# Kernel optimization log

Measured on AMD Instinct MI355X. Metric: run time of the kernel, lower is better.

Reference implementation:

```python
import jax, jax.numpy as jnp
import numpy as np
import math

N_FEATURES = 64
GAMMA_ORDER = 0.5
ALPHA, BETA, ETA = 0.3, 0.4, 0.3
MAX_K = 50


def _make_coeffs():
    # gamma_values[0] = Gamma(g+1); gamma_values[m] (m>=1) = Gamma(m)*Gamma(g-m+2)
    g0 = math.gamma(GAMMA_ORDER + 1.0)
    coeffs = np.zeros(MAX_K + 1, dtype=np.float32)
    coeffs[0] = 1.0
    for k in range(1, MAX_K + 1):
        gv_k = math.gamma(k) * math.gamma(GAMMA_ORDER - k + 2.0)
        coeffs[k] = ((-1.0) ** k) * g0 / gv_k
    return jnp.asarray(coeffs)


def setup_inputs() -> dict:
    key = jax.random.key(0)
    k1, k2, k3, k4 = jax.random.split(key, 4)
    B, T, F = 4, 8192, N_FEATURES
    x = jax.random.normal(k1, (B, T, F), dtype=jnp.float32)
    weight_matrix = jax.random.normal(k2, (F, F), dtype=jnp.float32)
    bound = 1.0 / math.sqrt(F)
    proj_w = jax.random.uniform(k3, (F, F), dtype=jnp.float32, minval=-bound, maxval=bound)
    proj_b = jax.random.uniform(k4, (F,), dtype=jnp.float32, minval=-bound, maxval=bound)
    kappa = jnp.float32(0.1)
    coeffs = _make_coeffs()
    return {"x": x, "weight_matrix": weight_matrix, "proj_w": proj_w,
            "proj_b": proj_b, "kappa": kappa, "coeffs": coeffs}


def _fractional_derivative(x, coeffs):
    # causal conv: result[:, t, :] = sum_{k=0}^{min(t, max_k)} coeffs[k] * x[:, t-k, :]
    K = coeffs.shape[0]
    F = x.shape[-1]
    # depthwise 1D cross-correlation; kernel reversed so it implements x[t-k]
    kern = jnp.tile(coeffs[::-1][:, None, None], (1, 1, F))  # [K, 1, F]
    return jax.lax.conv_general_dilated(
        x, kern, window_strides=(1,), padding=[(K - 1, 0)],
        dimension_numbers=("NWC", "WIO", "NWC"), feature_group_count=F)


def reference(x, weight_matrix, proj_w, proj_b, kappa, coeffs):
    B, T, F = x.shape
    # 1) memory term: fractional derivative (causal conv)
    memory_term = _fractional_derivative(x, coeffs)

    # 2) coupling term: sum_j w[i,j] * tanh(x_i - x_j) * sigmoid(|x_i| + |x_j|)
    #    diagonal contributes tanh(0)=0, matching the i != j skip in the original.
    w = jax.nn.softmax(weight_matrix, axis=1)                 # [F, F]
    xi = x[..., :, None]                                      # [B, T, F, 1]
    xj = x[..., None, :]                                      # [B, T, 1, F]
    c = jnp.tanh(xi - xj) * jax.nn.sigmoid(jnp.abs(xi) + jnp.abs(xj))  # [B,T,F,F]
    coupling_term = jnp.einsum("btij,ij->bti", c, w)

    # 3) global term: proj(x[:, t]) * sum_{s=0}^{t} exp(-kappa * s)
    proj = x @ proj_w.T + proj_b                               # [B, T, F]
    kernel_cumsum = jnp.cumsum(jnp.exp(-kappa * jnp.arange(T, dtype=x.dtype)))
    global_term = proj * kernel_cumsum[None, :, None]

    output = ALPHA * memory_term + BETA * coupling_term + ETA * global_term
    return (output, memory_term)
```

## Files before the change

kernel.cpp:

```cpp
#include <hip/hip_runtime.h>
#include <hip/hip_fp16.h>
#include <math.h>

#define TT 8192
#define FF 64

typedef float f32x4 __attribute__((ext_vector_type(4)));

__device__ __forceinline__ float rcpf(float x) { return __builtin_amdgcn_rcpf(x); }

__global__ void prep_kernel(const float* __restrict__ W, const float* __restrict__ PW,
                            float* __restrict__ wsmT, float* __restrict__ pwT) {
    const int lane = threadIdx.x;
    const int wv   = threadIdx.y;
    for (int it = 0; it < 16; ++it) {
        const int r = wv * 16 + it;
        float v = W[r * 64 + lane];
        float m = v;
        #pragma unroll
        for (int off = 32; off >= 1; off >>= 1)
            m = fmaxf(m, __shfl_xor(m, off, 64));
        float e = __expf(v - m);
        float s = e;
        #pragma unroll
        for (int off = 32; off >= 1; off >>= 1)
            s += __shfl_xor(s, off, 64);
        wsmT[lane * 64 + r] = e * rcpf(s);
        pwT[lane * 64 + r]  = PW[r * 64 + lane];
    }
}

__global__ __launch_bounds__(256, 2)
void mcao_main(const float* __restrict__ x,
               const float* __restrict__ wsmT,
               const float* __restrict__ pwT,
               const float* __restrict__ pb,
               const float* __restrict__ kap,
               const float* __restrict__ coeffs,
               float* __restrict__ out,
               float* __restrict__ memout) {
    __shared__ __align__(16) char smem[66304];
    float*   xs  = (float*)smem;
    float*   tS  = (float*)smem;
    __half2* ux  = (__half2*)(smem + 16640);
    float*   P2  = (float*)(smem + 16640);
    float*   wS  = (float*)(smem + 33536);
    float*   pwS = (float*)(smem + 49920);

    const int tid  = threadIdx.x;
    const int lane = tid & 63;
    const int wv   = tid >> 6;

    const int sw = ((int)blockIdx.x & 7) * 64 + ((int)blockIdx.x >> 3);
    const int b  = sw >> 7;
    const int t0 = (sw & 127) * 64;
    const float* xb = x + (size_t)b * TT * FF;

    for (int i4 = tid; i4 < 114 * 16; i4 += 256) {
        const int s = i4 >> 4, f4 = i4 & 15, t = t0 - 50 + s;
        f32x4 v = {0.f, 0.f, 0.f, 0.f};
        if (t >= 0) v = *(const f32x4*)(xb + (size_t)t * 64 + f4 * 4);
        *(f32x4*)(&xs[i4 * 4]) = v;
    }
    #pragma unroll
    for (int k = 0; k < 4; ++k) {
        ((f32x4*)wS)[tid + 256 * k]  = ((const f32x4*)wsmT)[tid + 256 * k];
        ((f32x4*)pwS)[tid + 256 * k] = ((const f32x4*)pwT)[tid + 256 * k];
    }
    __syncthreads();

    float macc[16];
    #pragma unroll
    for (int r = 0; r < 16; ++r) macc[r] = 0.f;
    #pragma unroll
    for (int s = 0; s < 66; ++s) {
        const float xv = xs[(16 * wv + s) * 64 + lane];
        #pragma unroll
        for (int r = 0; r < 16; ++r) {
            const int k = r + 50 - s;
            if (0 <= k && k <= 50) macc[r] = fmaf(coeffs[k], xv, macc[r]);
        }
    }
    #pragma unroll
    for (int r = 0; r < 16; ++r)
        memout[(size_t)(b * TT + t0 + 16 * wv + r) * 64 + lane] = macc[r];

    const int prow = tid >> 2, pfq = tid & 3;
    float tq[16], uq[16], xq[16];
    #pragma unroll
    for (int c4 = 0; c4 < 4; ++c4) {
        const f32x4 xv4 = *(const f32x4*)(&xs[(50 + prow) * 64 + pfq * 16 + c4 * 4]);
        #pragma unroll
        for (int q = 0; q < 4; ++q) {
            const float xi = xv4[q];
            tq[c4 * 4 + q] = fmaf(-2.f, rcpf(__expf(2.f * xi) + 1.f), 1.f);
            uq[c4 * 4 + q] = __expf(-fabsf(xi));
            xq[c4 * 4 + q] = xi;
        }
    }
    __syncthreads();
    #pragma unroll
    for (int c = 0; c < 16; ++c) {
        const int f = pfq * 16 + c;
        tS[f * 65 + prow] = tq[c];
        ux[f * 66 + prow] = __floats2half2_rn(uq[c], xq[c]);
    }
    __syncthreads();

    const int i0 = wv * 16;
    float ti[16], ui[16];
    #pragma unroll
    for (int i = 0; i < 16; ++i) {
        ti[i] = tS[(i0 + i) * 65 + lane];
        ui[i] = __low2float(ux[(i0 + i) * 66 + lane]);
    }

    float cacc[16], pacc[16];
    #pragma unroll
    for (int i = 0; i < 16; ++i) { cacc[i] = 0.f; pacc[i] = 0.f; }

    #pragma unroll 4
    for (int j = 0; j < 64; ++j) {
        const float  tj  = tS[j * 65 + lane];
        const __half2 uxj = ux[j * 66 + lane];
        const float  ujf = __low2float(uxj);
        const float  xjf = __high2float(uxj);
        f32x4 w4[4], p4[4];
        #pragma unroll
        for (int q = 0; q < 4; ++q) {
            w4[q] = *(const f32x4*)(&wS[j * 64 + i0 + 4 * q]);
            p4[q] = *(const f32x4*)(&pwS[j * 64 + i0 + 4 * q]);
        }
        #pragma unroll
        for (int i = 0; i < 16; ++i) {
            const float wij = w4[i >> 2][i & 3];
            const float pij = p4[i >> 2][i & 3];
            const float d1 = fmaf(-ti[i], tj, 1.f);
            const float d2 = fmaf( ui[i], ujf, 1.f);
            const float rr = rcpf(d1 * d2);
            cacc[i] = fmaf((ti[i] - tj) * wij, rr, cacc[i]);
            pacc[i] = fmaf(xjf, pij, pacc[i]);
        }
    }

    const float kappa = kap[0];
    const float ksum  = (1.f - __expf(-kappa * (float)(t0 + lane + 1))) *
                        rcpf(1.f - __expf(-kappa));
    __syncthreads();
    #pragma unroll
    for (int i = 0; i < 16; ++i)
        P2[(i0 + i) * 65 + lane] =
            fmaf(0.4f, cacc[i], 0.3f * (pacc[i] + pb[i0 + i]) * ksum);
    __syncthreads();

    #pragma unroll
    for (int r = 0; r < 16; ++r) {
        const int row = 16 * wv + r;
        out[(size_t)(b * TT + t0 + row) * 64 + lane] =
            fmaf(0.3f, macc[r], P2[lane * 65 + row]);
    }
}

extern "C" void kernel_launch(void* const* d_in, const int* in_sizes, int n_in,
                              void* d_out, int out_size, void* d_ws, size_t ws_size,
                              hipStream_t stream) {
    const float* x   = (const float*)d_in[0];
    const float* W   = (const float*)d_in[1];
    const float* PW  = (const float*)d_in[2];
    const float* pb  = (const float*)d_in[3];
    const float* kap = (const float*)d_in[4];
    const float* cf  = (const float*)d_in[5];

    float* out    = (float*)d_out;
    float* memout = out + (size_t)4 * TT * FF;

    float* wsmT = (float*)d_ws;
    float* pwT  = wsmT + 64 * 64;

    hipLaunchKernelGGL(prep_kernel, dim3(1), dim3(64, 4), 0, stream, W, PW, wsmT, pwT);
    hipLaunchKernelGGL(mcao_main, dim3(4 * (TT / 64)), dim3(256), 0, stream,
                       x, wsmT, pwT, pb, kap, cf, out, memout);
}
```

Before: 50.59 us.

## Halve time tile to 32 rows and store weight matrices as fp16 in LDS

Cuts the time tile per block from 64 to 32 rows, which doubles the grid, and remaps threads so each wave covers 8 output features for 32 timesteps, using both wave halves. The softmax weights and projection weights are now stored as half precision, shrinking LDS use so four blocks fit per CU. The aim is more occupancy and parallelism, at the price of recomputing a relatively larger 50-row halo per tile and lower precision on the weights.

```diff
diff --git a/kernel.cpp b/kernel.cpp
--- a/kernel.cpp
+++ b/kernel.cpp
@@ -4,13 +4,15 @@
 
 #define TT 8192
 #define FF 64
+#define TILE 32
+#define HALO 50
 
 typedef float f32x4 __attribute__((ext_vector_type(4)));
 
 __device__ __forceinline__ float rcpf(float x) { return __builtin_amdgcn_rcpf(x); }
 
 __global__ void prep_kernel(const float* __restrict__ W, const float* __restrict__ PW,
-                            float* __restrict__ wsmT, float* __restrict__ pwT) {
+                            __half* __restrict__ wsmH, __half* __restrict__ pwH) {
     const int lane = threadIdx.x;
     const int wv   = threadIdx.y;
     for (int it = 0; it < 16; ++it) {
@@ -25,71 +27,69 @@
         #pragma unroll
         for (int off = 32; off >= 1; off >>= 1)
             s += __shfl_xor(s, off, 64);
-        wsmT[lane * 64 + r] = e * rcpf(s);
-        pwT[lane * 64 + r]  = PW[r * 64 + lane];
+        wsmH[lane * 64 + r] = __float2half(e * rcpf(s));
+        pwH[lane * 64 + r]  = __float2half(PW[r * 64 + lane]);
     }
 }
 
-__global__ __launch_bounds__(256, 2)
+__global__ __launch_bounds__(256, 4)
 void mcao_main(const float* __restrict__ x,
-               const float* __restrict__ wsmT,
-               const float* __restrict__ pwT,
+               const __half* __restrict__ wsmH,
+               const __half* __restrict__ pwH,
                const float* __restrict__ pb,
                const float* __restrict__ kap,
                const float* __restrict__ coeffs,
                float* __restrict__ out,
                float* __restrict__ memout) {
-    __shared__ __align__(16) char smem[66304];
+    __shared__ __align__(16) char smem[37376];
     float*   xs  = (float*)smem;
     float*   tS  = (float*)smem;
-    __half2* ux  = (__half2*)(smem + 16640);
-    float*   P2  = (float*)(smem + 16640);
-    float*   wS  = (float*)(smem + 33536);
-    float*   pwS = (float*)(smem + 49920);
+    __half2* ux  = (__half2*)(smem + 8448);
+    float*   P2  = (float*)smem;
+    __half*  wS  = (__half*)(smem + 20992);
+    __half*  pwS = (__half*)(smem + 29184);
 
     const int tid  = threadIdx.x;
     const int lane = tid & 63;
     const int wv   = tid >> 6;
 
-    const int sw = ((int)blockIdx.x & 7) * 64 + ((int)blockIdx.x >> 3);
-    const int b  = sw >> 7;
-    const int t0 = (sw & 127) * 64;
+    const int sw = ((int)blockIdx.x & 7) * 128 + ((int)blockIdx.x >> 3);
+    const int b  = sw >> 8;
+    const int t0 = (sw & 255) * TILE;
     const float* xb = x + (size_t)b * TT * FF;
 
-    for (int i4 = tid; i4 < 114 * 16; i4 += 256) {
-        const int s = i4 >> 4, f4 = i4 & 15, t = t0 - 50 + s;
+    for (int i4 = tid; i4 < (TILE + HALO) * 16; i4 += 256) {
+        const int s = i4 >> 4, f4 = i4 & 15, t = t0 - HALO + s;
         f32x4 v = {0.f, 0.f, 0.f, 0.f};
         if (t >= 0) v = *(const f32x4*)(xb + (size_t)t * 64 + f4 * 4);
         *(f32x4*)(&xs[i4 * 4]) = v;
     }
     #pragma unroll
-    for (int k = 0; k < 4; ++k) {
-        ((f32x4*)wS)[tid + 256 * k]  = ((const f32x4*)wsmT)[tid + 256 * k];
-        ((f32x4*)pwS)[tid + 256 * k] = ((const f32x4*)pwT)[tid + 256 * k];
+    for (int k = 0; k < 2; ++k) {
+        ((f32x4*)wS)[tid + 256 * k]  = ((const f32x4*)wsmH)[tid + 256 * k];
+        ((f32x4*)pwS)[tid + 256 * k] = ((const f32x4*)pwH)[tid + 256 * k];
     }
     __syncthreads();
 
-    float macc[16];
+    float macc[8] = {0.f,0.f,0.f,0.f,0.f,0.f,0.f,0.f};
     #pragma unroll
-    for (int r = 0; r < 16; ++r) macc[r] = 0.f;
-    #pragma unroll
-    for (int s = 0; s < 66; ++s) {
-        const float xv = xs[(16 * wv + s) * 64 + lane];
+    for (int s = 0; s < 58; ++s) {
+        const float xv = xs[(8 * wv + s) * 64 + lane];
         #pragma unroll
-        for (int r = 0; r < 16; ++r) {
+        for (int r = 0; r < 8; ++r) {
             const int k = r + 50 - s;
             if (0 <= k && k <= 50) macc[r] = fmaf(coeffs[k], xv, macc[r]);
         }
     }
     #pragma unroll
-    for (int r = 0; r < 16; ++r)
-        memout[(size_t)(b * TT + t0 + 16 * wv + r) * 64 + lane] = macc[r];
+    for (int r = 0; r < 8; ++r)
+        memout[(size_t)(b * TT + t0 + 8 * wv + r) * 64 + lane] = macc[r];
 
-    const int prow = tid >> 2, pfq = tid & 3;
-    float tq[16], uq[16], xq[16];
+    const int prow = tid >> 3, pfq = tid & 7;
+    float tq[8], uq[8], xq[8];
     #pragma unroll
-    for (int c4 = 0; c4 < 4; ++c4) {
-        const f32x4 xv4 = *(const f32x4*)(&xs[(50 + prow) * 64 + pfq * 16 + c4 * 4]);
+    for (int c4 = 0; c4 < 2; ++c4) {
+        const f32x4 xv4 = *(const f32x4*)(&xs[(HALO + prow) * 64 + pfq * 8 + c4 * 4]);
         #pragma unroll
         for (int q = 0; q < 4; ++q) {
             const float xi = xv4[q];
@@ -100,64 +100,60 @@
     }
     __syncthreads();
     #pragma unroll
-    for (int c = 0; c < 16; ++c) {
-        const int f = pfq * 16 + c;
-        tS[f * 65 + prow] = tq[c];
-        ux[f * 66 + prow] = __floats2half2_rn(uq[c], xq[c]);
+    for (int c = 0; c < 8; ++c) {
+        const int f = pfq * 8 + c;
+        tS[f * 33 + prow] = tq[c];
+        ux[f * 34 + prow] = __floats2half2_rn(uq[c], xq[c]);
     }
     __syncthreads();
 
-    const int i0 = wv * 16;
-    float ti[16], ui[16];
+    const int r  = lane & 31;
+    const int h  = lane >> 5;
+    const int ib = wv * 16 + h * 8;
+    float ti[8], ui[8];
     #pragma unroll
-    for (int i = 0; i < 16; ++i) {
-        ti[i] = tS[(i0 + i) * 65 + lane];
-        ui[i] = __low2float(ux[(i0 + i) * 66 + lane]);
+    for (int q = 0; q < 8; ++q) {
+        ti[q] = tS[(ib + q) * 33 + r];
+        ui[q] = __low2float(ux[(ib + q) * 34 + r]);
     }
 
-    float cacc[16], pacc[16];
-    #pragma unroll
-    for (int i = 0; i < 16; ++i) { cacc[i] = 0.f; pacc[i] = 0.f; }
-
-    #pragma unroll 4
+    float cacc[8] = {0,0,0,0,0,0,0,0};
+    float pacc[8] = {0,0,0,0,0,0,0,0};
+    #pragma unroll 8
     for (int j = 0; j < 64; ++j) {
-        const float  tj  = tS[j * 65 + lane];
-        const __half2 uxj = ux[j * 66 + lane];
+        const float  tj  = tS[j * 33 + r];
+        const __half2 uxj = ux[j * 34 + r];
         const float  ujf = __low2float(uxj);
         const float  xjf = __high2float(uxj);
-        f32x4 w4[4], p4[4];
+        __half wh[8], ph[8];
+        *(f32x4*)wh = *(const f32x4*)(wS  + j * 64 + ib);
+        *(f32x4*)ph = *(const f32x4*)(pwS + j * 64 + ib);
         #pragma unroll
-        for (int q = 0; q < 4; ++q) {
-            w4[q] = *(const f32x4*)(&wS[j * 64 + i0 + 4 * q]);
-            p4[q] = *(const f32x4*)(&pwS[j * 64 + i0 + 4 * q]);
-        }
-        #pragma unroll
-        for (int i = 0; i < 16; ++i) {
-            const float wij = w4[i >> 2][i & 3];
-            const float pij = p4[i >> 2][i & 3];
-            const float d1 = fmaf(-ti[i], tj, 1.f);
-            const float d2 = fmaf( ui[i], ujf, 1.f);
+        for (int q = 0; q < 8; ++q) {
+            const float d1 = fmaf(-ti[q], tj, 1.f);
+            const float d2 = fmaf( ui[q], ujf, 1.f);
             const float rr = rcpf(d1 * d2);
-            cacc[i] = fmaf((ti[i] - tj) * wij, rr, cacc[i]);
-            pacc[i] = fmaf(xjf, pij, pacc[i]);
+            const float s  = (ti[q] - tj) * rr;
+            cacc[q] = fmaf(__half2float(wh[q]), s,   cacc[q]);
+            pacc[q] = fmaf(__half2float(ph[q]), xjf, pacc[q]);
         }
     }
 
     const float kappa = kap[0];
-    const float ksum  = (1.f - __expf(-kappa * (float)(t0 + lane + 1))) *
+    const float ksum  = (1.f - __expf(-kappa * (float)(t0 + r + 1))) *
                         rcpf(1.f - __expf(-kappa));
     __syncthreads();
     #pragma unroll
-    for (int i = 0; i < 16; ++i)
-        P2[(i0 + i) * 65 + lane] =
-            fmaf(0.4f, cacc[i], 0.3f * (pacc[i] + pb[i0 + i]) * ksum);
+    for (int q = 0; q < 8; ++q)
+        P2[(ib + q) * 33 + r] =
+            fmaf(0.4f, cacc[q], 0.3f * (pacc[q] + pb[ib + q]) * ksum);
     __syncthreads();
 
     #pragma unroll
-    for (int r = 0; r < 16; ++r) {
-        const int row = 16 * wv + r;
+    for (int rr = 0; rr < 8; ++rr) {
+        const int row = 8 * wv + rr;
         out[(size_t)(b * TT + t0 + row) * 64 + lane] =
-            fmaf(0.3f, macc[r], P2[lane * 65 + row]);
+            fmaf(0.3f, macc[rr], P2[lane * 33 + row]);
     }
 }
 
@@ -174,10 +170,10 @@
     float* out    = (float*)d_out;
     float* memout = out + (size_t)4 * TT * FF;
 
-    float* wsmT = (float*)d_ws;
-    float* pwT  = wsmT + 64 * 64;
+    __half* wsmH = (__half*)d_ws;
+    __half* pwH  = wsmH + 64 * 64;
 
-    hipLaunchKernelGGL(prep_kernel, dim3(1), dim3(64, 4), 0, stream, W, PW, wsmT, pwT);
-    hipLaunchKernelGGL(mcao_main, dim3(4 * (TT / 64)), dim3(256), 0, stream,
-                       x, wsmT, pwT, pb, kap, cf, out, memout);
+    hipLaunchKernelGGL(prep_kernel, dim3(1), dim3(64, 4), 0, stream, W, PW, wsmH, pwH);
+    hipLaunchKernelGGL(mcao_main, dim3(4 * (TT / TILE)), dim3(256), 0, stream,
+                       x, wsmH, pwH, pb, kap, cf, out, memout);
 }
```

After: 54.10 us. 7.0% more time.

## Use 1024-thread blocks with 4 rows per wave and packed FP32 math

Applied to the files above, without the earlier changes.

Each 64-row tile is now split across 16 waves instead of 4, so every wave handles 4 output features and 4 time rows. This cuts per-thread register use and raises occupancy for the coupling loop. The coupling loop now uses packed two-wide FMAs, and tanh plus packed half-precision u/x values share one interleaved shared-memory layout, so a single 8-byte load fetches them together. In exchange, the causal convolution re-reads more halo rows per output row (54 loads per 4 rows instead of 66 per 16), and the launch-bounds hint asks for more resident waves than the hardware can hold.

```diff
diff --git a/kernel.cpp b/kernel.cpp
--- a/kernel.cpp
+++ b/kernel.cpp
@@ -4,7 +4,10 @@
 
 #define TT 8192
 #define FF 64
+#define TILE 64
+#define HALO 50
 
+typedef float f32x2 __attribute__((ext_vector_type(2)));
 typedef float f32x4 __attribute__((ext_vector_type(4)));
 
 __device__ __forceinline__ float rcpf(float x) { return __builtin_amdgcn_rcpf(x); }
@@ -30,7 +33,7 @@
     }
 }
 
-__global__ __launch_bounds__(256, 2)
+__global__ __launch_bounds__(1024, 8)
 void mcao_main(const float* __restrict__ x,
                const float* __restrict__ wsmT,
                const float* __restrict__ pwT,
@@ -39,13 +42,12 @@
                const float* __restrict__ coeffs,
                float* __restrict__ out,
                float* __restrict__ memout) {
-    __shared__ __align__(16) char smem[66304];
-    float*   xs  = (float*)smem;
-    float*   tS  = (float*)smem;
-    __half2* ux  = (__half2*)(smem + 16640);
-    float*   P2  = (float*)(smem + 16640);
-    float*   wS  = (float*)(smem + 33536);
-    float*   pwS = (float*)(smem + 49920);
+    __shared__ __align__(16) char smem[66048];
+    float* xs  = (float*)smem;
+    f32x2* tux = (f32x2*)smem;
+    float* P2  = (float*)smem;
+    float* wS  = (float*)(smem + 33280);
+    float* pwS = (float*)(smem + 49664);
 
     const int tid  = threadIdx.x;
     const int lane = tid & 63;
@@ -53,111 +55,113 @@
 
     const int sw = ((int)blockIdx.x & 7) * 64 + ((int)blockIdx.x >> 3);
     const int b  = sw >> 7;
-    const int t0 = (sw & 127) * 64;
+    const int t0 = (sw & 127) * TILE;
     const float* xb = x + (size_t)b * TT * FF;
 
-    for (int i4 = tid; i4 < 114 * 16; i4 += 256) {
-        const int s = i4 >> 4, f4 = i4 & 15, t = t0 - 50 + s;
-        f32x4 v = {0.f, 0.f, 0.f, 0.f};
-        if (t >= 0) v = *(const f32x4*)(xb + (size_t)t * 64 + f4 * 4);
-        *(f32x4*)(&xs[i4 * 4]) = v;
+    #pragma unroll
+    for (int k = 0; k < 2; ++k) {
+        const int i4 = tid + 1024 * k;
+        if (i4 < 114 * 16) {
+            const int s = i4 >> 4, f4 = i4 & 15, t = t0 - HALO + s;
+            f32x4 v = {0.f, 0.f, 0.f, 0.f};
+            if (t >= 0) v = *(const f32x4*)(xb + (size_t)t * 64 + f4 * 4);
+            *(f32x4*)(&xs[s * 64 + f4 * 4]) = v;
+        }
     }
-    #pragma unroll
-    for (int k = 0; k < 4; ++k) {
-        ((f32x4*)wS)[tid + 256 * k]  = ((const f32x4*)wsmT)[tid + 256 * k];
-        ((f32x4*)pwS)[tid + 256 * k] = ((const f32x4*)pwT)[tid + 256 * k];
-    }
+    ((f32x4*)wS)[tid]  = ((const f32x4*)wsmT)[tid];
+    ((f32x4*)pwS)[tid] = ((const f32x4*)pwT)[tid];
     __syncthreads();
 
-    float macc[16];
+    float macc[4] = {0.f, 0.f, 0.f, 0.f};
     #pragma unroll
-    for (int r = 0; r < 16; ++r) macc[r] = 0.f;
-    #pragma unroll
-    for (int s = 0; s < 66; ++s) {
-        const float xv = xs[(16 * wv + s) * 64 + lane];
+    for (int s = 0; s < 54; ++s) {
+        const float xv = xs[(4 * wv + s) * 64 + lane];
         #pragma unroll
-        for (int r = 0; r < 16; ++r) {
+        for (int r = 0; r < 4; ++r) {
             const int k = r + 50 - s;
             if (0 <= k && k <= 50) macc[r] = fmaf(coeffs[k], xv, macc[r]);
         }
     }
     #pragma unroll
-    for (int r = 0; r < 16; ++r)
-        memout[(size_t)(b * TT + t0 + 16 * wv + r) * 64 + lane] = macc[r];
+    for (int r = 0; r < 4; ++r)
+        memout[(size_t)(b * TT + t0 + 4 * wv + r) * 64 + lane] = macc[r];
 
-    const int prow = tid >> 2, pfq = tid & 3;
-    float tq[16], uq[16], xq[16];
+    const int erow = tid >> 4, f0 = (tid & 15) * 4;
+    const f32x4 xv4 = *(const f32x4*)(&xs[(HALO + erow) * 64 + f0]);
+    float tq[4]; unsigned pk[4];
     #pragma unroll
-    for (int c4 = 0; c4 < 4; ++c4) {
-        const f32x4 xv4 = *(const f32x4*)(&xs[(50 + prow) * 64 + pfq * 16 + c4 * 4]);
-        #pragma unroll
-        for (int q = 0; q < 4; ++q) {
-            const float xi = xv4[q];
-            tq[c4 * 4 + q] = fmaf(-2.f, rcpf(__expf(2.f * xi) + 1.f), 1.f);
-            uq[c4 * 4 + q] = __expf(-fabsf(xi));
-            xq[c4 * 4 + q] = xi;
-        }
+    for (int q = 0; q < 4; ++q) {
+        const float xi = xv4[q];
+        tq[q] = fmaf(-2.f, rcpf(__expf(2.f * xi) + 1.f), 1.f);
+        const float uu = __expf(-fabsf(xi));
+        pk[q] = (unsigned)__half_as_ushort(__float2half_rn(xi)) << 16 |
+                (unsigned)__half_as_ushort(__float2half_rn(uu));
     }
     __syncthreads();
     #pragma unroll
-    for (int c = 0; c < 16; ++c) {
-        const int f = pfq * 16 + c;
-        tS[f * 65 + prow] = tq[c];
-        ux[f * 66 + prow] = __floats2half2_rn(uq[c], xq[c]);
+    for (int q = 0; q < 4; ++q) {
+        f32x2 e; e.x = tq[q]; e.y = __uint_as_float(pk[q]);
+        tux[(f0 + q) * 65 + erow] = e;
     }
     __syncthreads();
 
-    const int i0 = wv * 16;
-    float ti[16], ui[16];
+    const int r  = lane;
+    const int ib = __builtin_amdgcn_readfirstlane(wv) * 4;
+
+    f32x2 tiP[2], uiP[2];
     #pragma unroll
-    for (int i = 0; i < 16; ++i) {
-        ti[i] = tS[(i0 + i) * 65 + lane];
-        ui[i] = __low2float(ux[(i0 + i) * 66 + lane]);
+    for (int q = 0; q < 4; ++q) {
+        const f32x2 e = tux[(ib + q) * 65 + r];
+        const unsigned u = __float_as_uint(e.y);
+        tiP[q >> 1][q & 1] = e.x;
+        uiP[q >> 1][q & 1] = __half2float(__ushort_as_half((unsigned short)(u & 0xFFFF)));
     }
 
-    float cacc[16], pacc[16];
-    #pragma unroll
-    for (int i = 0; i < 16; ++i) { cacc[i] = 0.f; pacc[i] = 0.f; }
-
-    #pragma unroll 4
+    f32x2 cac[2] = {{0.f, 0.f}, {0.f, 0.f}};
+    f32x2 pac[2] = {{0.f, 0.f}, {0.f, 0.f}};
+    const f32x2 one2 = {1.f, 1.f};
+    #pragma unroll 8
     for (int j = 0; j < 64; ++j) {
-        const float  tj  = tS[j * 65 + lane];
-        const __half2 uxj = ux[j * 66 + lane];
-        const float  ujf = __low2float(uxj);
-        const float  xjf = __high2float(uxj);
-        f32x4 w4[4], p4[4];
+        const f32x2 e = tux[j * 65 + r];
+        const unsigned u = __float_as_uint(e.y);
+        const float tj = e.x;
+        const float uj = __half2float(__ushort_as_half((unsigned short)(u & 0xFFFF)));
+        const float xj = __half2float(__ushort_as_half((unsigned short)(u >> 16)));
+        const f32x4 w4 = *(const f32x4*)(wS  + j * 64 + ib);
+        const f32x4 p4 = *(const f32x4*)(pwS + j * 64 + ib);
+        const f32x2 tjj = {tj, tj}, ujj = {uj, uj}, xjj = {xj, xj};
         #pragma unroll
-        for (int q = 0; q < 4; ++q) {
-            w4[q] = *(const f32x4*)(&wS[j * 64 + i0 + 4 * q]);
-            p4[q] = *(const f32x4*)(&pwS[j * 64 + i0 + 4 * q]);
-        }
-        #pragma unroll
-        for (int i = 0; i < 16; ++i) {
-            const float wij = w4[i >> 2][i & 3];
-            const float pij = p4[i >> 2][i & 3];
-            const float d1 = fmaf(-ti[i], tj, 1.f);
-            const float d2 = fmaf( ui[i], ujf, 1.f);
-            const float rr = rcpf(d1 * d2);
-            cacc[i] = fmaf((ti[i] - tj) * wij, rr, cacc[i]);
-            pacc[i] = fmaf(xjf, pij, pacc[i]);
+        for (int g = 0; g < 2; ++g) {
+            const f32x2 d1  = __builtin_elementwise_fma(-tiP[g], tjj, one2);
+            const f32x2 d2  = __builtin_elementwise_fma( uiP[g], ujj, one2);
+            const f32x2 den = d1 * d2;
+            f32x2 rr; rr.x = rcpf(den.x); rr.y = rcpf(den.y);
+            const f32x2 s = (tiP[g] - tjj) * rr;
+            f32x2 wg; wg.x = w4[2 * g]; wg.y = w4[2 * g + 1];
+            f32x2 pg; pg.x = p4[2 * g]; pg.y = p4[2 * g + 1];
+            cac[g] = __builtin_elementwise_fma(s,   wg, cac[g]);
+            pac[g] = __builtin_elementwise_fma(xjj, pg, pac[g]);
         }
     }
 
-    const float kappa = kap[0];
-    const float ksum  = (1.f - __expf(-kappa * (float)(t0 + lane + 1))) *
-                        rcpf(1.f - __expf(-kappa));
+    const float kappa  = kap[0];
+    const float inv1mr = rcpf(1.f - __expf(-kappa));
+    const float ksum   = (1.f - __expf(-kappa * (float)(t0 + r + 1))) * inv1mr;
+    const f32x4 pbv    = *(const f32x4*)(pb + ib);
     __syncthreads();
     #pragma unroll
-    for (int i = 0; i < 16; ++i)
-        P2[(i0 + i) * 65 + lane] =
-            fmaf(0.4f, cacc[i], 0.3f * (pacc[i] + pb[i0 + i]) * ksum);
+    for (int q = 0; q < 4; ++q) {
+        const float cv = (q & 1) ? cac[q >> 1].y : cac[q >> 1].x;
+        const float pv = (q & 1) ? pac[q >> 1].y : pac[q >> 1].x;
+        P2[(ib + q) * 65 + r] = fmaf(0.4f, cv, 0.3f * (pv + pbv[q]) * ksum);
+    }
     __syncthreads();
 
     #pragma unroll
-    for (int r = 0; r < 16; ++r) {
-        const int row = 16 * wv + r;
+    for (int rr2 = 0; rr2 < 4; ++rr2) {
+        const int row = 4 * wv + rr2;
         out[(size_t)(b * TT + t0 + row) * 64 + lane] =
-            fmaf(0.3f, macc[r], P2[lane * 65 + row]);
+            fmaf(0.3f, macc[rr2], P2[lane * 65 + row]);
     }
 }
 
@@ -178,6 +182,6 @@
     float* pwT  = wsmT + 64 * 64;
 
     hipLaunchKernelGGL(prep_kernel, dim3(1), dim3(64, 4), 0, stream, W, PW, wsmT, pwT);
-    hipLaunchKernelGGL(mcao_main, dim3(4 * (TT / 64)), dim3(256), 0, stream,
+    hipLaunchKernelGGL(mcao_main, dim3(4 * (TT / TILE)), dim3(1024), 0, stream,
                        x, wsmT, pwT, pb, kap, cf, out, memout);
 }
```

Result: faster. 48.42 us (-4.3%).
